# Optimization experiments

Measured on AMD Instinct MI355X. Metric: run time of the kernel, lower is better.

## Reference

```python
import jax, jax.numpy as jnp
import numpy as np
import math

H_HEADS = 16
D_PER = 64
D_MODEL = 1024
B, L = 8, 1024


def _dual_attention(q1, k1, q2, k2, v):
    # all [B,h,L,d]; scores = avg of two scaled QK^T
    scale = 1.0 / math.sqrt(q1.shape[-1])
    s1 = jnp.einsum('bhqd,bhkd->bhqk', q1, k1) * scale
    s2 = jnp.einsum('bhqd,bhkd->bhqk', q2, k2) * scale
    p = jax.nn.softmax((s1 + s2) * 0.5, axis=-1)
    return jnp.einsum('bhqk,bhkd->bhqd', p, v)


def _proj(X, W, b):
    # [B,L,D] -> [B,h,L,d]
    Bb, Ll, _ = X.shape
    y = X @ W + b
    return y.reshape(Bb, Ll, H_HEADS, D_PER).transpose(0, 2, 1, 3)


def _mha(Q1, K1, Q2, K2, V, Wq, bq, Wk, bk, Wv, bv, Wo, bo):
    q1 = _proj(Q1, Wq, bq)
    k1 = _proj(K1, Wk, bk)
    q2 = _proj(Q2, Wq, bq)  # same linear as q1 (linears[0])
    k2 = _proj(K2, Wk, bk)  # same linear as k1 (linears[1])
    v = _proj(V, Wv, bv)
    o = _dual_attention(q1, k1, q2, k2, v)  # [B,h,L,d]
    Bb = o.shape[0]
    o = o.transpose(0, 2, 1, 3).reshape(Bb, -1, H_HEADS * D_PER)
    return o @ Wo + bo  # [B,L,D]


def setup_inputs() -> dict:
    key = jax.random.key(0)
    ks = jax.random.split(key, 5)
    sc = 1.0 / math.sqrt(D_MODEL)
    return {
        'x': jax.random.normal(ks[0], (B, L, 3, D_MODEL), jnp.float32),
        'Wq': jax.random.normal(ks[1], (D_MODEL, H_HEADS * D_PER), jnp.float32) * sc,
        'bq': jnp.zeros((H_HEADS * D_PER,), jnp.float32),
        'Wk': jax.random.normal(ks[2], (D_MODEL, H_HEADS * D_PER), jnp.float32) * sc,
        'bk': jnp.zeros((H_HEADS * D_PER,), jnp.float32),
        'Wv': jax.random.normal(ks[3], (D_MODEL, H_HEADS * D_PER), jnp.float32) * sc,
        'bv': jnp.zeros((H_HEADS * D_PER,), jnp.float32),
        'Wo': jax.random.normal(ks[4], (H_HEADS * D_PER, D_MODEL), jnp.float32) * sc,
        'bo': jnp.zeros((D_MODEL,), jnp.float32),
    }


def reference(x, Wq, bq, Wk, bk, Wv, bv, Wo, bo):
    Hx = x[:, :, 0, :]
    Tx = x[:, :, 1, :]
    Rx = x[:, :, 2, :]
    p = (Wq, bq, Wk, bk, Wv, bv, Wo, bo)
    H_new = _mha(Tx, Tx, Rx, Rx, Hx, *p)
    T_new = _mha(Hx, Hx, Rx, Rx, Tx, *p)
    R_new = _mha(Hx, Hx, Tx, Tx, Rx, *p)
    return jnp.stack([H_new, T_new, R_new], axis=2)  # [B,L,3,D]
```

## Files before the change

kernel.cpp:

```cpp
#include <hip/hip_runtime.h>
#include <hip/hip_bf16.h>
#include <stdint.h>

#define NTOK 8192
#define DM   1024

typedef __bf16 bf16x8 __attribute__((ext_vector_type(8)));
typedef float  f32x4  __attribute__((ext_vector_type(4)));

__device__ __forceinline__ unsigned short f2bf(float f) {
  union { float f; unsigned u; } v; v.f = f;
  unsigned r = v.u + 0x7FFFu + ((v.u >> 16) & 1u);
  return (unsigned short)(r >> 16);
}

__device__ __forceinline__ void gld16(const void* g, const void* l) {
  __builtin_amdgcn_global_load_lds(
      (const __attribute__((address_space(1))) uint32_t*)g,
      (__attribute__((address_space(3))) uint32_t*)l, 16, 0, 0);
}

__global__ void convert_x(const float* __restrict__ x, unsigned short* __restrict__ Xbf) {
  int idx = (blockIdx.x * 256 + threadIdx.x) * 4;
  int s   = idx >> 23;
  int rem = idx & ((1 << 23) - 1);
  int tok = rem >> 10;
  int d   = rem & 1023;
  const float4 v = *(const float4*)&x[((size_t)tok * 3 + s) * 1024 + d];
  ushort4 o;
  o.x = f2bf(v.x); o.y = f2bf(v.y); o.z = f2bf(v.z); o.w = f2bf(v.w);
  *(ushort4*)&Xbf[idx] = o;
}

__global__ void transpose_w(const float* __restrict__ W, unsigned short* __restrict__ Wt) {
  __shared__ float t[32][33];
  int tx = threadIdx.x, ty = threadIdx.y;
  int bx = blockIdx.x * 32, by = blockIdx.y * 32;
#pragma unroll
  for (int i = 0; i < 32; i += 8)
    t[ty + i][tx] = W[(size_t)(by + ty + i) * 1024 + bx + tx];
  __syncthreads();
#pragma unroll
  for (int i = 0; i < 32; i += 8)
    Wt[(size_t)(bx + ty + i) * 1024 + by + tx] = f2bf(t[tx][ty + i]);
}

#define STG_A(tt, d, hf) do { \
  gld16(Ag + (size_t)((hf) * 128) * 1024 + (tt) * 64,      &lds[((d)*2+(hf))*8192 + wave*512]); \
  gld16(Ag + (size_t)((hf) * 128 + 64) * 1024 + (tt) * 64, &lds[((d)*2+(hf))*8192 + wave*512 + 4096]); \
} while (0)
#define STG_B(tt, d, hf) do { \
  gld16(Bg + (size_t)((hf) * 128) * 1024 + (tt) * 64,      &lds[32768 + ((d)*2+(hf))*8192 + wave*512]); \
  gld16(Bg + (size_t)((hf) * 128 + 64) * 1024 + (tt) * 64, &lds[32768 + ((d)*2+(hf))*8192 + wave*512 + 4096]); \
} while (0)
#define RD_AG(g, d) do { \
  const unsigned short* _p = &lds[((d)*2 + wm) * 8192]; \
  _Pragma("unroll") for (int m2 = 0; m2 < 4; ++m2) \
  _Pragma("unroll") for (int ks = 0; ks < 2; ++ks) \
    af[(g)*4 + m2][ks] = *(const bf16x8*)&_p[((g)*4 + m2)*1024 + l16*64 + (((ks*4 + quad) ^ sw8) * 8)]; \
} while (0)
#define RD_BG(g, d) do { \
  const unsigned short* _p = &lds[32768 + ((d)*2 + (wn >> 1)) * 8192 + (wn & 1) * 4096]; \
  _Pragma("unroll") for (int n2 = 0; n2 < 2; ++n2) \
  _Pragma("unroll") for (int ks = 0; ks < 2; ++ks) \
    bfr[(g)*2 + n2][ks] = *(const bf16x8*)&_p[((g)*2 + n2)*1024 + l16*64 + (((ks*4 + quad) ^ sw8) * 8)]; \
} while (0)
#define MM_Q(qm, qn) do { \
  __builtin_amdgcn_s_setprio(1); \
  _Pragma("unroll") for (int m2 = 0; m2 < 4; ++m2) \
  _Pragma("unroll") for (int n2 = 0; n2 < 2; ++n2) \
  _Pragma("unroll") for (int ks = 0; ks < 2; ++ks) \
    acc[(qm)*4 + m2][(qn)*2 + n2] = __builtin_amdgcn_mfma_f32_16x16x32_bf16( \
      af[(qm)*4 + m2][ks], bfr[(qn)*2 + n2][ks], acc[(qm)*4 + m2][(qn)*2 + n2], 0, 0, 0); \
  __builtin_amdgcn_s_setprio(0); \
} while (0)
#define PBAR() do { __builtin_amdgcn_s_barrier(); __builtin_amdgcn_sched_barrier(0); } while (0)
#define WLGK0() do { asm volatile("s_waitcnt lgkmcnt(0)" ::: "memory"); __builtin_amdgcn_sched_barrier(0); } while (0)

__device__ __forceinline__ void gemm256_core(
    const unsigned short* __restrict__ A, const unsigned short* __restrict__ Bt,
    unsigned short* lds, f32x4 acc[8][4], int m0, int n0)
{
  int tid = threadIdx.x;
  int wave = tid >> 6, lane = tid & 63, quad = lane >> 4, l16 = lane & 15;
  int wm = wave >> 2, wn = wave & 3;
  int sw8 = l16 & 7;
  int srow = wave * 8 + (lane >> 3);
  int schk = ((lane & 7) ^ (lane >> 3)) * 8;
  const unsigned short* Ag = A  + (size_t)(m0 + srow) * 1024 + schk;
  const unsigned short* Bg = Bt + (size_t)(n0 + srow) * 1024 + schk;
  bf16x8 af[8][2], bfr[4][2];

  STG_A(0, 0, 0); STG_A(0, 0, 1); STG_B(0, 0, 0); STG_B(0, 0, 1);
  STG_A(1, 1, 0); STG_A(1, 1, 1); STG_B(1, 1, 0);
  asm volatile("s_waitcnt vmcnt(6)" ::: "memory");
  PBAR();

  for (int t = 0; t < 16; t += 2) {
    RD_AG(0, 0); RD_BG(0, 0);
    STG_B(t + 1, 1, 1);
    __builtin_amdgcn_s_barrier(); WLGK0();
    MM_Q(0, 0);
    PBAR();
    RD_AG(1, 0);
    __builtin_amdgcn_s_barrier(); WLGK0();
    MM_Q(1, 0);
    PBAR();
    RD_BG(1, 0);
    if (t + 2 < 16) { STG_A(t + 2, 0, 0); STG_A(t + 2, 0, 1); }
    __builtin_amdgcn_s_barrier(); WLGK0();
    MM_Q(0, 1);
    PBAR();
    if (t + 2 < 16) STG_B(t + 2, 0, 0);
    __builtin_amdgcn_s_barrier(); __builtin_amdgcn_sched_barrier(0);
    MM_Q(1, 1);
    if (t + 2 < 16) { asm volatile("s_waitcnt vmcnt(6)" ::: "memory"); }
    else            { asm volatile("s_waitcnt vmcnt(0)" ::: "memory"); }
    PBAR();
    RD_AG(0, 1); RD_BG(0, 1);
    if (t + 2 < 16) STG_B(t + 2, 0, 1);
    __builtin_amdgcn_s_barrier(); WLGK0();
    MM_Q(0, 0);
    PBAR();
    RD_AG(1, 1);
    __builtin_amdgcn_s_barrier(); WLGK0();
    MM_Q(1, 0);
    PBAR();
    RD_BG(1, 1);
    if (t + 3 < 16) { STG_A(t + 3, 1, 0); STG_A(t + 3, 1, 1); }
    __builtin_amdgcn_s_barrier(); WLGK0();
    MM_Q(0, 1);
    PBAR();
    if (t + 3 < 16) STG_B(t + 3, 1, 0);
    __builtin_amdgcn_s_barrier(); __builtin_amdgcn_sched_barrier(0);
    MM_Q(1, 1);
    if (t + 3 < 16) { asm volatile("s_waitcnt vmcnt(6)" ::: "memory"); }
    PBAR();
  }
}

__global__ __launch_bounds__(512, 2) void gemm_proj(
    const unsigned short* __restrict__ Xbf, const unsigned short* __restrict__ Wt,
    unsigned short* __restrict__ P,
    const float* __restrict__ bq, const float* __restrict__ bk, const float* __restrict__ bv)
{
  __shared__ alignas(16) unsigned short lds[65536];
  int z = blockIdx.z, s = z / 3, w = z - s * 3;
  const float* bias = (w == 0) ? bq : (w == 1) ? bk : bv;
  int f = blockIdx.x;
  int swz = (f & 7) * 16 + (f >> 3);
  int m0 = (swz & 31) * 256, n0 = (swz >> 5) * 256;
  f32x4 acc[8][4];
#pragma unroll
  for (int i = 0; i < 8; i++)
#pragma unroll
    for (int j = 0; j < 4; j++) acc[i][j] = (f32x4){0.f, 0.f, 0.f, 0.f};
  gemm256_core(Xbf + (size_t)s * NTOK * 1024, Wt + (size_t)w * 1048576, lds, acc, m0, n0);

  int tid = threadIdx.x, wave = tid >> 6, lane = tid & 63, quad = lane >> 4, l16 = lane & 15;
  int wm = wave >> 2, wn = wave & 3;
  int rbase = m0 + wm * 128, cbase = n0 + wn * 64;
  unsigned short* C = P + (size_t)z * NTOK * 1024;
  if (w == 2) {
#pragma unroll
    for (int mi = 0; mi < 8; mi++) {
      int row0 = rbase + mi * 16 + quad * 4;
      int b = row0 >> 10, l0 = row0 & 1023;
#pragma unroll
      for (int ni = 0; ni < 4; ni++) {
        int col = cbase + ni * 16 + l16;
        float bcol = bias[col];
        int hh = col >> 6, d = col & 63;
        ushort4 o4;
        o4.x = f2bf(acc[mi][ni][0] + bcol);
        o4.y = f2bf(acc[mi][ni][1] + bcol);
        o4.z = f2bf(acc[mi][ni][2] + bcol);
        o4.w = f2bf(acc[mi][ni][3] + bcol);
        *(ushort4*)&C[(size_t)(b * 16 + hh) * 65536 + (size_t)d * 1024 + l0] = o4;
      }
    }
  } else {
#pragma unroll
    for (int mi = 0; mi < 8; mi++)
#pragma unroll
      for (int ni = 0; ni < 4; ni++) {
        int col = cbase + ni * 16 + l16;
        float bcol = bias[col];
#pragma unroll
        for (int r = 0; r < 4; r++) {
          int row = rbase + mi * 16 + quad * 4 + r;
          C[(size_t)row * 1024 + col] = f2bf(acc[mi][ni][r] + bcol);
        }
      }
  }
}

__global__ __launch_bounds__(512, 2) void gemm_out(
    const unsigned short* __restrict__ Oattn, const unsigned short* __restrict__ WtO,
    float* __restrict__ out, const float* __restrict__ bo)
{
  __shared__ alignas(16) unsigned short lds[65536];
  int s = blockIdx.z;
  int f = blockIdx.x;
  int swz = (f & 7) * 16 + (f >> 3);
  int m0 = (swz & 31) * 256, n0 = (swz >> 5) * 256;
  f32x4 acc[8][4];
#pragma unroll
  for (int i = 0; i < 8; i++)
#pragma unroll
    for (int j = 0; j < 4; j++) acc[i][j] = (f32x4){0.f, 0.f, 0.f, 0.f};
  gemm256_core(Oattn + (size_t)s * NTOK * 1024, WtO, lds, acc, m0, n0);

  int tid = threadIdx.x, wave = tid >> 6, lane = tid & 63, quad = lane >> 4, l16 = lane & 15;
  int wm = wave >> 2, wn = wave & 3;
  int rbase = m0 + wm * 128, cbase = n0 + wn * 64;
#pragma unroll
  for (int mi = 0; mi < 8; mi++)
#pragma unroll
    for (int ni = 0; ni < 4; ni++) {
      int col = cbase + ni * 16 + l16;
      float bcol = bo[col];
#pragma unroll
      for (int r = 0; r < 4; r++) {
        int row = rbase + mi * 16 + quad * 4 + r;
        out[(size_t)row * 3072 + s * 1024 + col] = acc[mi][ni][r] + bcol;
      }
    }
}

__global__ __launch_bounds__(256, 4) void attn(
    const unsigned short* __restrict__ P, unsigned short* __restrict__ Oa)
{
  __shared__ alignas(16) unsigned short lK1[64 * 64];
  __shared__ alignas(16) unsigned short lK2[64 * 64];
  __shared__ alignas(16) unsigned short lV [64 * 64];
  __shared__ alignas(16) unsigned short pls[4][32 * 40];
  int o  = blockIdx.z;
  int As = (o == 0) ? 1 : 0;
  int Bs = (o == 2) ? 1 : 2;
  int b = blockIdx.x >> 4, h = blockIdx.x & 15;
  int tid = threadIdx.x, wave = tid >> 6, lane = tid & 63, quad = lane >> 4, l16 = lane & 15;
  int q0 = blockIdx.y * 128 + wave * 32;
  size_t bh_off = (size_t)b * 1024 * 1024 + h * 64;
  const unsigned short* Q1 = P + (size_t)(As * 3 + 0) * NTOK * 1024 + bh_off;
  const unsigned short* K1 = P + (size_t)(As * 3 + 1) * NTOK * 1024 + bh_off;
  const unsigned short* Q2 = P + (size_t)(Bs * 3 + 0) * NTOK * 1024 + bh_off;
  const unsigned short* K2 = P + (size_t)(Bs * 3 + 1) * NTOK * 1024 + bh_off;
  const unsigned short* V  = P + (size_t)(o * 3 + 2) * NTOK * 1024
                               + (size_t)(b * 16 + h) * 65536;
  unsigned short* myp = pls[wave];

  bf16x8 q1f[2][2], q2f[2][2];
#pragma unroll
  for (int qt = 0; qt < 2; qt++)
#pragma unroll
    for (int c = 0; c < 2; c++) {
      q1f[qt][c] = *(const bf16x8*)&Q1[(size_t)(q0 + qt * 16 + l16) * 1024 + c * 32 + quad * 8];
      q2f[qt][c] = *(const bf16x8*)&Q2[(size_t)(q0 + qt * 16 + l16) * 1024 + c * 32 + quad * 8];
    }
  bf16x8 ones;
#pragma unroll
  for (int j = 0; j < 8; j++) ones[j] = (__bf16)1.0f;

  int r8 = lane >> 3;
  int cs = ((lane & 7) ^ r8) * 8;
  int srow = wave * 16 + r8;
  const unsigned short* K1s = K1 + (size_t)srow * 1024 + cs;
  const unsigned short* K2s = K2 + (size_t)srow * 1024 + cs;
  const unsigned short* Vs  = V  + (size_t)srow * 1024 + cs;
  int fsw = (l16 & 7);

  f32x4 oacc[2][4];
#pragma unroll
  for (int qt = 0; qt < 2; qt++)
#pragma unroll
    for (int dt = 0; dt < 4; dt++) oacc[qt][dt] = (f32x4){0.f, 0.f, 0.f, 0.f};
  f32x4 lsum[2];
  lsum[0] = (f32x4){0.f, 0.f, 0.f, 0.f};
  lsum[1] = (f32x4){0.f, 0.f, 0.f, 0.f};

  const float SC = 0.09016844136867f;

  for (int k0 = 0; k0 < 1024; k0 += 64) {
#pragma unroll
    for (int half = 0; half < 2; half++) {
      size_t krow = (size_t)(k0 + half * 8) * 1024;
      gld16(K1s + krow,                 lK1 + (wave * 16 + half * 8) * 64);
      gld16(K2s + krow,                 lK2 + (wave * 16 + half * 8) * 64);
      gld16(Vs + k0 + half * 8 * 1024,  lV  + (wave * 16 + half * 8) * 64);
    }
    __syncthreads();

#pragma unroll
    for (int kc = 0; kc < 2; kc++) {
      f32x4 sacc[2][2];
      sacc[0][0] = (f32x4){0.f, 0.f, 0.f, 0.f};
      sacc[0][1] = (f32x4){0.f, 0.f, 0.f, 0.f};
      sacc[1][0] = (f32x4){0.f, 0.f, 0.f, 0.f};
      sacc[1][1] = (f32x4){0.f, 0.f, 0.f, 0.f};
      __builtin_amdgcn_s_setprio(1);
#pragma unroll
      for (int kt = 0; kt < 2; kt++) {
        int krow = (kc * 32 + kt * 16 + l16) * 64;
        bf16x8 k1a = *(const bf16x8*)&lK1[krow + ((quad ^ fsw) * 8)];
        bf16x8 k1b = *(const bf16x8*)&lK1[krow + (((quad + 4) ^ fsw) * 8)];
        bf16x8 k2a = *(const bf16x8*)&lK2[krow + ((quad ^ fsw) * 8)];
        bf16x8 k2b = *(const bf16x8*)&lK2[krow + (((quad + 4) ^ fsw) * 8)];
#pragma unroll
        for (int qt = 0; qt < 2; qt++) {
          sacc[qt][kt] = __builtin_amdgcn_mfma_f32_16x16x32_bf16(q1f[qt][0], k1a, sacc[qt][kt], 0, 0, 0);
          sacc[qt][kt] = __builtin_amdgcn_mfma_f32_16x16x32_bf16(q1f[qt][1], k1b, sacc[qt][kt], 0, 0, 0);
          sacc[qt][kt] = __builtin_amdgcn_mfma_f32_16x16x32_bf16(q2f[qt][0], k2a, sacc[qt][kt], 0, 0, 0);
          sacc[qt][kt] = __builtin_amdgcn_mfma_f32_16x16x32_bf16(q2f[qt][1], k2b, sacc[qt][kt], 0, 0, 0);
        }
      }
      __builtin_amdgcn_s_setprio(0);
#pragma unroll
      for (int qt = 0; qt < 2; qt++)
#pragma unroll
        for (int kt = 0; kt < 2; kt++)
#pragma unroll
          for (int r2 = 0; r2 < 2; r2++) {
            union { float f; unsigned u; } e0, e1;
            e0.f = __builtin_amdgcn_exp2f(sacc[qt][kt][r2 * 2]     * SC);
            e1.f = __builtin_amdgcn_exp2f(sacc[qt][kt][r2 * 2 + 1] * SC);
            unsigned pk = __builtin_amdgcn_perm(e1.u + 0x8000u, e0.u + 0x8000u, 0x07060302u);
            int row = qt * 16 + quad * 4 + r2 * 2;
            myp[row * 40 + kt * 16 + l16]       = (unsigned short)pk;
            myp[(row + 1) * 40 + kt * 16 + l16] = (unsigned short)(pk >> 16);
          }
      bf16x8 pa0 = *(const bf16x8*)&myp[l16 * 40 + quad * 8];
      bf16x8 pa1 = *(const bf16x8*)&myp[(16 + l16) * 40 + quad * 8];
      __builtin_amdgcn_s_setprio(1);
      lsum[0] = __builtin_amdgcn_mfma_f32_16x16x32_bf16(pa0, ones, lsum[0], 0, 0, 0);
      lsum[1] = __builtin_amdgcn_mfma_f32_16x16x32_bf16(pa1, ones, lsum[1], 0, 0, 0);
#pragma unroll
      for (int dt = 0; dt < 4; dt++) {
        bf16x8 vf = *(const bf16x8*)&lV[(dt * 16 + l16) * 64 + (((kc * 4 + quad) ^ fsw) * 8)];
        oacc[0][dt] = __builtin_amdgcn_mfma_f32_16x16x32_bf16(pa0, vf, oacc[0][dt], 0, 0, 0);
        oacc[1][dt] = __builtin_amdgcn_mfma_f32_16x16x32_bf16(pa1, vf, oacc[1][dt], 0, 0, 0);
      }
      __builtin_amdgcn_s_setprio(0);
    }
    __syncthreads();
  }

  unsigned short* Od = Oa + (size_t)o * NTOK * 1024 + bh_off;
#pragma unroll
  for (int qt = 0; qt < 2; qt++) {
    f32x4 inv;
#pragma unroll
    for (int r = 0; r < 4; r++) inv[r] = 1.0f / lsum[qt][r];
#pragma unroll
    for (int dt = 0; dt < 4; dt++)
#pragma unroll
      for (int r = 0; r < 4; r++) {
        float val = oacc[qt][dt][r] * inv[r];
        Od[(size_t)(q0 + qt * 16 + quad * 4 + r) * 1024 + dt * 16 + l16] = f2bf(val);
      }
  }
}

extern "C" void kernel_launch(void* const* d_in, const int* in_sizes, int n_in,
                              void* d_out, int out_size, void* d_ws, size_t ws_size,
                              hipStream_t stream) {
  (void)in_sizes; (void)n_in; (void)out_size; (void)ws_size;
  const float* x  = (const float*)d_in[0];
  const float* Wq = (const float*)d_in[1];
  const float* bq = (const float*)d_in[2];
  const float* Wk = (const float*)d_in[3];
  const float* bk = (const float*)d_in[4];
  const float* Wv = (const float*)d_in[5];
  const float* bv = (const float*)d_in[6];
  const float* Wo = (const float*)d_in[7];
  const float* bo = (const float*)d_in[8];
  float* out = (float*)d_out;

  char* ws = (char*)d_ws;
  unsigned short* Xbf = (unsigned short*)(ws + 0);
  unsigned short* Wt  = (unsigned short*)(ws + 50331648);
  unsigned short* P   = (unsigned short*)(ws + 58720256);
  unsigned short* Oa  = (unsigned short*)(ws + 209715200);

  convert_x<<<24576, 256, 0, stream>>>(x, Xbf);
  dim3 tb(32, 8), tg(32, 32);
  transpose_w<<<tg, tb, 0, stream>>>(Wq, Wt + 0 * 1048576);
  transpose_w<<<tg, tb, 0, stream>>>(Wk, Wt + 1 * 1048576);
  transpose_w<<<tg, tb, 0, stream>>>(Wv, Wt + 2 * 1048576);
  transpose_w<<<tg, tb, 0, stream>>>(Wo, Wt + 3 * 1048576);

  gemm_proj<<<dim3(128, 1, 9), 512, 0, stream>>>(Xbf, Wt, P, bq, bk, bv);
  attn<<<dim3(128, 8, 3), 256, 0, stream>>>(P, Oa);
  gemm_out<<<dim3(128, 1, 3), 512, 0, stream>>>(Oa, Wt + 3 * 1048576, out, bo);
}
```

Before: 613.5 us.

## Restructure GEMM pipeline, fold softmax scale into Q projection, merge weight transposes

Replaces the GEMM core's two-stage, half-tile staged schedule with a simpler per-K-tile double-buffered loop. It keeps fewer A fragments live (af reduced from 8x2 to 4x2) and drops the explicit lgkmcnt waits between quadrant MFMAs. It folds the attention scale (log2e/sqrt(d)) into the Q projection epilogue so the attention kernel no longer multiplies each score before exp2. It also merges the four weight-transpose launches into one launch. These changes aim to cut register pressure, per-score ALU work and launch overhead, at the risk of worse load/compute overlap in the GEMM and bf16 rounding of the pre-scaled Q.

```diff
diff --git a/kernel.cpp b/kernel.cpp
--- a/kernel.cpp
+++ b/kernel.cpp
@@ -32,8 +32,13 @@
   *(ushort4*)&Xbf[idx] = o;
 }
 
-__global__ void transpose_w(const float* __restrict__ W, unsigned short* __restrict__ Wt) {
+__global__ void transpose_w4(const float* __restrict__ W0, const float* __restrict__ W1,
+                             const float* __restrict__ W2, const float* __restrict__ W3,
+                             unsigned short* __restrict__ Wt) {
   __shared__ float t[32][33];
+  int z = blockIdx.z;
+  const float* W = (z == 0) ? W0 : (z == 1) ? W1 : (z == 2) ? W2 : W3;
+  unsigned short* D = Wt + (size_t)z * 1048576;
   int tx = threadIdx.x, ty = threadIdx.y;
   int bx = blockIdx.x * 32, by = blockIdx.y * 32;
 #pragma unroll
@@ -42,40 +47,30 @@
   __syncthreads();
 #pragma unroll
   for (int i = 0; i < 32; i += 8)
-    Wt[(size_t)(bx + ty + i) * 1024 + by + tx] = f2bf(t[tx][ty + i]);
-}
-
-#define STG_A(tt, d, hf) do { \
-  gld16(Ag + (size_t)((hf) * 128) * 1024 + (tt) * 64,      &lds[((d)*2+(hf))*8192 + wave*512]); \
-  gld16(Ag + (size_t)((hf) * 128 + 64) * 1024 + (tt) * 64, &lds[((d)*2+(hf))*8192 + wave*512 + 4096]); \
-} while (0)
-#define STG_B(tt, d, hf) do { \
-  gld16(Bg + (size_t)((hf) * 128) * 1024 + (tt) * 64,      &lds[32768 + ((d)*2+(hf))*8192 + wave*512]); \
-  gld16(Bg + (size_t)((hf) * 128 + 64) * 1024 + (tt) * 64, &lds[32768 + ((d)*2+(hf))*8192 + wave*512 + 4096]); \
-} while (0)
-#define RD_AG(g, d) do { \
-  const unsigned short* _p = &lds[((d)*2 + wm) * 8192]; \
+    D[(size_t)(bx + ty + i) * 1024 + by + tx] = f2bf(t[tx][ty + i]);
+}
+
+#define STGA(tt) do { _Pragma("unroll") for (int j = 0; j < 4; ++j) \
+  gld16(Ag + (size_t)(j * 64) * 1024 + (tt) * 64, &lds[(((tt) & 1) * 16384) + j * 4096 + wave * 512]); } while (0)
+#define STGB(tt) do { _Pragma("unroll") for (int j = 0; j < 4; ++j) \
+  gld16(Bg + (size_t)(j * 64) * 1024 + (tt) * 64, &lds[32768 + (((tt) & 1) * 16384) + j * 4096 + wave * 512]); } while (0)
+#define RDAF(g, tt) do { \
+  const unsigned short* _p = &lds[(((tt) & 1) * 16384) + (wm * 128 + (g) * 64) * 64]; \
   _Pragma("unroll") for (int m2 = 0; m2 < 4; ++m2) \
   _Pragma("unroll") for (int ks = 0; ks < 2; ++ks) \
-    af[(g)*4 + m2][ks] = *(const bf16x8*)&_p[((g)*4 + m2)*1024 + l16*64 + (((ks*4 + quad) ^ sw8) * 8)]; \
-} while (0)
-#define RD_BG(g, d) do { \
-  const unsigned short* _p = &lds[32768 + ((d)*2 + (wn >> 1)) * 8192 + (wn & 1) * 4096]; \
+    af[m2][ks] = *(const bf16x8*)&_p[(m2 * 16 + l16) * 64 + (((ks * 4 + quad) ^ sw8) * 8)]; } while (0)
+#define RDBF(h, tt) do { \
+  const unsigned short* _p = &lds[32768 + (((tt) & 1) * 16384) + (wn * 64 + (h) * 32) * 64]; \
   _Pragma("unroll") for (int n2 = 0; n2 < 2; ++n2) \
   _Pragma("unroll") for (int ks = 0; ks < 2; ++ks) \
-    bfr[(g)*2 + n2][ks] = *(const bf16x8*)&_p[((g)*2 + n2)*1024 + l16*64 + (((ks*4 + quad) ^ sw8) * 8)]; \
-} while (0)
-#define MM_Q(qm, qn) do { \
-  __builtin_amdgcn_s_setprio(1); \
+    bfr[(h) * 2 + n2][ks] = *(const bf16x8*)&_p[(n2 * 16 + l16) * 64 + (((ks * 4 + quad) ^ sw8) * 8)]; } while (0)
+#define MMQ(g, h) do { __builtin_amdgcn_s_setprio(1); \
   _Pragma("unroll") for (int m2 = 0; m2 < 4; ++m2) \
   _Pragma("unroll") for (int n2 = 0; n2 < 2; ++n2) \
   _Pragma("unroll") for (int ks = 0; ks < 2; ++ks) \
-    acc[(qm)*4 + m2][(qn)*2 + n2] = __builtin_amdgcn_mfma_f32_16x16x32_bf16( \
-      af[(qm)*4 + m2][ks], bfr[(qn)*2 + n2][ks], acc[(qm)*4 + m2][(qn)*2 + n2], 0, 0, 0); \
-  __builtin_amdgcn_s_setprio(0); \
-} while (0)
-#define PBAR() do { __builtin_amdgcn_s_barrier(); __builtin_amdgcn_sched_barrier(0); } while (0)
-#define WLGK0() do { asm volatile("s_waitcnt lgkmcnt(0)" ::: "memory"); __builtin_amdgcn_sched_barrier(0); } while (0)
+    acc[(g) * 4 + m2][(h) * 2 + n2] = __builtin_amdgcn_mfma_f32_16x16x32_bf16( \
+      af[m2][ks], bfr[(h) * 2 + n2][ks], acc[(g) * 4 + m2][(h) * 2 + n2], 0, 0, 0); \
+  __builtin_amdgcn_s_setprio(0); } while (0)
 
 __device__ __forceinline__ void gemm256_core(
     const unsigned short* __restrict__ A, const unsigned short* __restrict__ Bt,
@@ -89,53 +84,34 @@
   int schk = ((lane & 7) ^ (lane >> 3)) * 8;
   const unsigned short* Ag = A  + (size_t)(m0 + srow) * 1024 + schk;
   const unsigned short* Bg = Bt + (size_t)(n0 + srow) * 1024 + schk;
-  bf16x8 af[8][2], bfr[4][2];
-
-  STG_A(0, 0, 0); STG_A(0, 0, 1); STG_B(0, 0, 0); STG_B(0, 0, 1);
-  STG_A(1, 1, 0); STG_A(1, 1, 1); STG_B(1, 1, 0);
-  asm volatile("s_waitcnt vmcnt(6)" ::: "memory");
-  PBAR();
-
-  for (int t = 0; t < 16; t += 2) {
-    RD_AG(0, 0); RD_BG(0, 0);
-    STG_B(t + 1, 1, 1);
-    __builtin_amdgcn_s_barrier(); WLGK0();
-    MM_Q(0, 0);
-    PBAR();
-    RD_AG(1, 0);
-    __builtin_amdgcn_s_barrier(); WLGK0();
-    MM_Q(1, 0);
-    PBAR();
-    RD_BG(1, 0);
-    if (t + 2 < 16) { STG_A(t + 2, 0, 0); STG_A(t + 2, 0, 1); }
-    __builtin_amdgcn_s_barrier(); WLGK0();
-    MM_Q(0, 1);
-    PBAR();
-    if (t + 2 < 16) STG_B(t + 2, 0, 0);
-    __builtin_amdgcn_s_barrier(); __builtin_amdgcn_sched_barrier(0);
-    MM_Q(1, 1);
-    if (t + 2 < 16) { asm volatile("s_waitcnt vmcnt(6)" ::: "memory"); }
-    else            { asm volatile("s_waitcnt vmcnt(0)" ::: "memory"); }
-    PBAR();
-    RD_AG(0, 1); RD_BG(0, 1);
-    if (t + 2 < 16) STG_B(t + 2, 0, 1);
-    __builtin_amdgcn_s_barrier(); WLGK0();
-    MM_Q(0, 0);
-    PBAR();
-    RD_AG(1, 1);
-    __builtin_amdgcn_s_barrier(); WLGK0();
-    MM_Q(1, 0);
-    PBAR();
-    RD_BG(1, 1);
-    if (t + 3 < 16) { STG_A(t + 3, 1, 0); STG_A(t + 3, 1, 1); }
-    __builtin_amdgcn_s_barrier(); WLGK0();
-    MM_Q(0, 1);
-    PBAR();
-    if (t + 3 < 16) STG_B(t + 3, 1, 0);
-    __builtin_amdgcn_s_barrier(); __builtin_amdgcn_sched_barrier(0);
-    MM_Q(1, 1);
-    if (t + 3 < 16) { asm volatile("s_waitcnt vmcnt(6)" ::: "memory"); }
-    PBAR();
+  bf16x8 af[4][2], bfr[4][2];
+
+  STGA(0); STGB(0); STGA(1);
+  asm volatile("s_waitcnt vmcnt(4)" ::: "memory");
+  __builtin_amdgcn_s_barrier();
+  __builtin_amdgcn_sched_barrier(0);
+
+  for (int t = 0; t < 16; ++t) {
+    RDAF(0, t); RDBF(0, t);
+    if (t + 1 < 16) STGB(t + 1);
+    __builtin_amdgcn_s_barrier();
+    MMQ(0, 0);
+    __builtin_amdgcn_s_barrier();
+    RDBF(1, t);
+    __builtin_amdgcn_s_barrier();
+    MMQ(0, 1);
+    __builtin_amdgcn_s_barrier();
+    RDAF(1, t);
+    __builtin_amdgcn_s_barrier();
+    MMQ(1, 0);
+    __builtin_amdgcn_s_barrier();
+    if (t + 2 < 16) STGA(t + 2);
+    __builtin_amdgcn_s_barrier();
+    MMQ(1, 1);
+    if (t + 2 < 16)      { asm volatile("s_waitcnt vmcnt(4)" ::: "memory"); }
+    else if (t == 14)    { asm volatile("s_waitcnt vmcnt(0)" ::: "memory"); }
+    __builtin_amdgcn_s_barrier();
+    __builtin_amdgcn_sched_barrier(0);
   }
 }
 
@@ -147,6 +123,7 @@
   __shared__ alignas(16) unsigned short lds[65536];
   int z = blockIdx.z, s = z / 3, w = z - s * 3;
   const float* bias = (w == 0) ? bq : (w == 1) ? bk : bv;
+  float osc = (w == 0) ? 0.09016844136867f : 1.0f;
   int f = blockIdx.x;
   int swz = (f & 7) * 16 + (f >> 3);
   int m0 = (swz & 31) * 256, n0 = (swz >> 5) * 256;
@@ -189,7 +166,7 @@
 #pragma unroll
         for (int r = 0; r < 4; r++) {
           int row = rbase + mi * 16 + quad * 4 + r;
-          C[(size_t)row * 1024 + col] = f2bf(acc[mi][ni][r] + bcol);
+          C[(size_t)row * 1024 + col] = f2bf((acc[mi][ni][r] + bcol) * osc);
         }
       }
   }
@@ -279,8 +256,6 @@
   lsum[0] = (f32x4){0.f, 0.f, 0.f, 0.f};
   lsum[1] = (f32x4){0.f, 0.f, 0.f, 0.f};
 
-  const float SC = 0.09016844136867f;
-
   for (int k0 = 0; k0 < 1024; k0 += 64) {
 #pragma unroll
     for (int half = 0; half < 2; half++) {
@@ -322,8 +297,8 @@
 #pragma unroll
           for (int r2 = 0; r2 < 2; r2++) {
             union { float f; unsigned u; } e0, e1;
-            e0.f = __builtin_amdgcn_exp2f(sacc[qt][kt][r2 * 2]     * SC);
-            e1.f = __builtin_amdgcn_exp2f(sacc[qt][kt][r2 * 2 + 1] * SC);
+            e0.f = __builtin_amdgcn_exp2f(sacc[qt][kt][r2 * 2]);
+            e1.f = __builtin_amdgcn_exp2f(sacc[qt][kt][r2 * 2 + 1]);
             unsigned pk = __builtin_amdgcn_perm(e1.u + 0x8000u, e0.u + 0x8000u, 0x07060302u);
             int row = qt * 16 + quad * 4 + r2 * 2;
             myp[row * 40 + kt * 16 + l16]       = (unsigned short)pk;
@@ -383,11 +358,7 @@
   unsigned short* Oa  = (unsigned short*)(ws + 209715200);
 
   convert_x<<<24576, 256, 0, stream>>>(x, Xbf);
-  dim3 tb(32, 8), tg(32, 32);
-  transpose_w<<<tg, tb, 0, stream>>>(Wq, Wt + 0 * 1048576);
-  transpose_w<<<tg, tb, 0, stream>>>(Wk, Wt + 1 * 1048576);
-  transpose_w<<<tg, tb, 0, stream>>>(Wv, Wt + 2 * 1048576);
-  transpose_w<<<tg, tb, 0, stream>>>(Wo, Wt + 3 * 1048576);
+  transpose_w4<<<dim3(32, 32, 4), dim3(32, 8), 0, stream>>>(Wq, Wk, Wv, Wo, Wt);
 
   gemm_proj<<<dim3(128, 1, 9), 512, 0, stream>>>(Xbf, Wt, P, bq, bk, bv);
   attn<<<dim3(128, 8, 3), 256, 0, stream>>>(P, Oa);
```

Result: faster. 601.0 us (-2.0%).
